# Kernel optimization log

Hardware: AMD Instinct MI355X
Metric: run time of the kernel (lower is better)

Reference implementation:

```python
import jax, jax.numpy as jnp
import numpy as np

HEAD_SIZE = 64  # EMBEDDING_SIZE(384) // HEAD_NO(6)

def setup_inputs() -> dict:
    key = jax.random.key(0)
    ks = jax.random.split(key, 6)
    B, T, C, H, D = 256, 256, 384, 6, 64
    s = 0.02
    return {
        "x": jax.random.normal(ks[0], (B, T, C), dtype=jnp.float32),
        "Wq": jax.random.normal(ks[1], (H, C, D), dtype=jnp.float32) * s,
        "Wk": jax.random.normal(ks[2], (H, C, D), dtype=jnp.float32) * s,
        "Wv": jax.random.normal(ks[3], (H, C, D), dtype=jnp.float32) * s,
        "Wproj": jax.random.normal(ks[4], (C, C), dtype=jnp.float32) * s,
        "bproj": jnp.zeros((C,), dtype=jnp.float32),
    }

def reference(x, Wq, Wk, Wv, Wproj, bproj):
    B, T, C = x.shape
    # per-head projections, stacked over heads h: [B, H, T, D]
    q = jnp.einsum('btc,hcd->bhtd', x, Wq)
    k = jnp.einsum('btc,hcd->bhtd', x, Wk)
    v = jnp.einsum('btc,hcd->bhtd', x, Wv)
    scale = 1.0 / jnp.sqrt(jnp.asarray(HEAD_SIZE, dtype=x.dtype))
    # scores [B, H, T, T]; causal mask (masked_fill then /scale == scale then mask, since -inf/scale=-inf)
    scores = jnp.einsum('bhtd,bhsd->bhts', q, k) * scale
    causal = jnp.tril(jnp.ones((T, T), dtype=bool))
    scores = jnp.where(causal, scores, -jnp.inf)
    w = jax.nn.softmax(scores, axis=-1)
    # dropout is identity in eval mode
    out = jnp.einsum('bhts,bhsd->bhtd', w, v)          # [B, H, T, D]
    out = out.transpose(0, 2, 1, 3).reshape(B, T, C)    # concat heads -> [B, T, C]
    return out @ Wproj + bproj
```

## Files before the change

kernel.cpp:

```cpp
#include <hip/hip_runtime.h>
#include <hip/hip_bf16.h>

typedef __bf16 bf16;
typedef unsigned int u32;
typedef __attribute__((ext_vector_type(8))) __bf16 bf16x8;
typedef __attribute__((ext_vector_type(4))) float f32x4;

#define Bsz 256
#define Tsz 256
#define Csz 384
#define Hn  6
#define Dh  64
#define NQKV 1152

#define MFMA16(a, b, c) __builtin_amdgcn_mfma_f32_16x16x32_bf16(a, b, c, 0, 0, 0)

typedef __attribute__((address_space(3))) u32 lds_u32;
typedef __attribute__((address_space(1))) const u32 gbl_u32;
__device__ __forceinline__ void gl2lds16(const void* g, void* l) {
    __builtin_amdgcn_global_load_lds((gbl_u32*)g, (lds_u32*)l, 16, 0, 0);
}

__device__ __forceinline__ float redmax16(float x) {
    x = fmaxf(x, __shfl_xor(x, 1));
    x = fmaxf(x, __shfl_xor(x, 2));
    x = fmaxf(x, __shfl_xor(x, 4));
    x = fmaxf(x, __shfl_xor(x, 8));
    return x;
}
__device__ __forceinline__ float redsum16(float x) {
    x += __shfl_xor(x, 1);
    x += __shfl_xor(x, 2);
    x += __shfl_xor(x, 4);
    x += __shfl_xor(x, 8);
    return x;
}

__global__ __launch_bounds__(256) void convert_x(
    const float* __restrict__ x, bf16* __restrict__ xb)
{
    size_t i = ((size_t)blockIdx.x * 256 + threadIdx.x) * 8;
    float4 f0 = *(const float4*)&x[i];
    float4 f1 = *(const float4*)&x[i + 4];
    bf16x8 o;
    o[0] = (bf16)f0.x; o[1] = (bf16)f0.y; o[2] = (bf16)f0.z; o[3] = (bf16)f0.w;
    o[4] = (bf16)f1.x; o[5] = (bf16)f1.y; o[6] = (bf16)f1.z; o[7] = (bf16)f1.w;
    *(bf16x8*)&xb[i] = o;
}

__global__ __launch_bounds__(384) void prep_w(
    const float* __restrict__ Wq, const float* __restrict__ Wk,
    const float* __restrict__ Wv, const float* __restrict__ Wp,
    bf16* __restrict__ Btqkv, bf16* __restrict__ Bpt)
{
    const int n = blockIdx.x, k = threadIdx.x;
    if (n < NQKV) {
        int wi = n / Csz, rem = n - wi * Csz, h = rem >> 6, d = rem & 63;
        const float* W = wi == 0 ? Wq : (wi == 1 ? Wk : Wv);
        Btqkv[(size_t)n * Csz + k] = (bf16)W[((size_t)h * Csz + k) * Dh + d];
    } else {
        int n2 = n - NQKV;
        Bpt[(size_t)n2 * Csz + k] = (bf16)Wp[(size_t)k * Csz + n2];
    }
}


__device__ __forceinline__ void stage_tile(
    const char* Ab, const char* Bb, int m0, int n0, int t,
    bf16 (*As)[256][64], bf16 (*Bs)[128][64], int buf, int tid)
{
    const int srow = tid >> 3;
    const int scs  = ((tid & 7) * 16) ^ (((tid >> 3) & 7) << 4);
    #pragma unroll
    for (int j = 0; j < 8; ++j)
        gl2lds16(Ab + (size_t)(m0 + j * 32 + srow) * 768 + t * 128 + scs,
                 (char*)&As[buf][0][0] + j * 4096 + tid * 16);
    #pragma unroll
    for (int j = 0; j < 4; ++j)
        gl2lds16(Bb + (size_t)(n0 + j * 32 + srow) * 768 + t * 128 + scs,
                 (char*)&Bs[buf][0][0] + j * 4096 + tid * 16);
}

__device__ __forceinline__ void compute_tile(
    const bf16 (*As)[256][64], const bf16 (*Bs)[128][64], int buf,
    int wmw, int wnw, int l4, int quad, f32x4 acc[8][4])
{
    const char* Ap = (const char*)&As[buf][0][0];
    const char* Bp = (const char*)&Bs[buf][0][0];
    const int cswz = (l4 & 7) << 4;
    bf16x8 bfr[4][2];
    #pragma unroll
    for (int fn = 0; fn < 4; ++fn)
        #pragma unroll
        for (int ks = 0; ks < 2; ++ks)
            bfr[fn][ks] = *(const bf16x8*)(Bp + (wnw * 64 + fn * 16 + l4) * 128 +
                                           ((ks * 64 + quad * 16) ^ cswz));
    #pragma unroll
    for (int mh = 0; mh < 2; ++mh) {
        bf16x8 af[4][2];
        #pragma unroll
        for (int fr = 0; fr < 4; ++fr)
            #pragma unroll
            for (int ks = 0; ks < 2; ++ks)
                af[fr][ks] = *(const bf16x8*)(Ap + (wmw * 128 + mh * 64 + fr * 16 + l4) * 128 +
                                              ((ks * 64 + quad * 16) ^ cswz));
        __builtin_amdgcn_s_setprio(1);
        #pragma unroll
        for (int ks = 0; ks < 2; ++ks)
            #pragma unroll
            for (int fr = 0; fr < 4; ++fr)
                #pragma unroll
                for (int fn = 0; fn < 4; ++fn)
                    acc[mh * 4 + fr][fn] = MFMA16(af[fr][ks], bfr[fn][ks], acc[mh * 4 + fr][fn]);
        __builtin_amdgcn_s_setprio(0);
    }
}

#define GEMM_PIPE()                                                            \
    stage_tile(Ab, Bb, m0, n0, 0, As, Bs, 0, tid);                             \
    stage_tile(Ab, Bb, m0, n0, 1, As, Bs, 1, tid);                             \
    asm volatile("s_waitcnt vmcnt(12)" ::: "memory");                          \
    __builtin_amdgcn_s_barrier();                                              \
    _Pragma("unroll")                                                          \
    for (int t = 0; t < 6; ++t) {                                              \
        if (t < 4) stage_tile(Ab, Bb, m0, n0, t + 2, As, Bs, (t + 2) % 3, tid);\
        compute_tile(As, Bs, t % 3, wmw, wnw, l4, quad, acc);                  \
        if (t < 4) {                                                           \
            asm volatile("s_waitcnt vmcnt(12)" ::: "memory");                  \
            __builtin_amdgcn_s_barrier();                                      \
        } else if (t == 4) {                                                   \
            asm volatile("s_waitcnt vmcnt(0)" ::: "memory");                   \
            __builtin_amdgcn_s_barrier();                                      \
        }                                                                      \
    }

__global__ __launch_bounds__(256, 1) void qkv_gemm(
    const bf16* __restrict__ A, const bf16* __restrict__ Bt,
    bf16* __restrict__ q, bf16* __restrict__ k, bf16* __restrict__ v)
{
    __shared__ bf16 As[3][256][64];
    __shared__ bf16 Bs[3][128][64];
    const int tid = threadIdx.x, w = tid >> 6, lane = tid & 63;
    const int l4 = lane & 15, quad = lane >> 4;
    const int wmw = w >> 1, wnw = w & 1;

    const int orig = blockIdx.x;
    const int id = (orig & 7) * 288 + (orig >> 3);
    const int mt_ = id / 9, nt_ = id - mt_ * 9;
    const int m0 = mt_ * 256, n0 = nt_ * 128;

    const char* Ab = (const char*)A;
    const char* Bb = (const char*)Bt;
    f32x4 acc[8][4] = {};

    GEMM_PIPE();

    #pragma unroll
    for (int fn = 0; fn < 4; ++fn) {
        int n = n0 + wnw * 64 + fn * 16 + l4;
        int wi = n / Csz, rem = n - wi * Csz;
        int h = rem >> 6, d = rem & 63;
        bf16* outp = wi == 0 ? q : (wi == 1 ? k : v);
        #pragma unroll
        for (int fr = 0; fr < 8; ++fr)
            #pragma unroll
            for (int r = 0; r < 4; ++r) {
                int m = m0 + wmw * 128 + fr * 16 + quad * 4 + r;
                int b = m >> 8, tt = m & 255;
                outp[(((size_t)(b * Hn + h)) * Tsz + tt) * Dh + d] = (bf16)acc[fr][fn][r];
            }
    }
}

__global__ __launch_bounds__(256, 1) void proj_gemm(
    const bf16* __restrict__ A, const bf16* __restrict__ Bt,
    const float* __restrict__ bias, float* __restrict__ out)
{
    __shared__ bf16 As[3][256][64];
    __shared__ bf16 Bs[3][128][64];
    const int tid = threadIdx.x, w = tid >> 6, lane = tid & 63;
    const int l4 = lane & 15, quad = lane >> 4;
    const int wmw = w >> 1, wnw = w & 1;

    const int orig = blockIdx.x;
    const int id = (orig & 7) * 96 + (orig >> 3);
    const int mt_ = id / 3, nt_ = id - mt_ * 3;
    const int m0 = mt_ * 256, n0 = nt_ * 128;

    const char* Ab = (const char*)A;
    const char* Bb = (const char*)Bt;
    f32x4 acc[8][4] = {};

    GEMM_PIPE();

    #pragma unroll
    for (int fn = 0; fn < 4; ++fn) {
        int n = n0 + wnw * 64 + fn * 16 + l4;
        float bv = bias[n];
        #pragma unroll
        for (int fr = 0; fr < 8; ++fr)
            #pragma unroll
            for (int r = 0; r < 4; ++r) {
                int m = m0 + wmw * 128 + fr * 16 + quad * 4 + r;
                out[(size_t)m * Csz + n] = acc[fr][fn][r] + bv;
            }
    }
}

__global__ __launch_bounds__(256) void attn_mfma(
    const bf16* __restrict__ q, const bf16* __restrict__ k, const bf16* __restrict__ v,
    bf16* __restrict__ att)
{
    __shared__ bf16 Kl[64][72];
    __shared__ bf16 Vt[64][72];
    __shared__ bf16 Pl[4][16][72];
    const float SCL = 0.18033688f;
    const int tid = threadIdx.x, w = tid >> 6, lane = tid & 63;
    const int l4 = lane & 15, quad = lane >> 4;

    const int orig = blockIdx.x;
    const int blk = (orig & 7) * 768 + (orig >> 3);
    const int bh = blk >> 2, qt = blk & 3;
    const int b = bh / Hn, h = bh % Hn;
    const bf16* qb = q + (size_t)bh * Tsz * Dh;
    const bf16* kb = k + (size_t)bh * Tsz * Dh;
    const bf16* vb = v + (size_t)bh * Tsz * Dh;

    const int trow = qt * 64 + w * 16 + l4;
    const bf16x8 qa0 = *(const bf16x8*)&qb[trow * Dh + quad * 8];
    const bf16x8 qa1 = *(const bf16x8*)&qb[trow * Dh + 32 + quad * 8];

    f32x4 o[4] = {f32x4{0,0,0,0}, f32x4{0,0,0,0}, f32x4{0,0,0,0}, f32x4{0,0,0,0}};
    float mrun[4] = {-3.0e38f, -3.0e38f, -3.0e38f, -3.0e38f};
    float lrun[4] = {0.f, 0.f, 0.f, 0.f};

    for (int kt = 0; kt <= qt; ++kt) {
        #pragma unroll
        for (int it = 0; it < 2; ++it) {
            int idx = it * 256 + tid;
            int s = idx >> 3, d8 = (idx & 7) * 8;
            *(bf16x8*)&Kl[s][d8] = *(const bf16x8*)&kb[(kt * 64 + s) * Dh + d8];
        }
        #pragma unroll
        for (int it = 0; it < 2; ++it) {
            int idx = it * 256 + tid;
            int s = idx & 63, d8 = (idx >> 6) * 8;
            bf16x8 vv = *(const bf16x8*)&vb[(kt * 64 + s) * Dh + d8];
            #pragma unroll
            for (int j = 0; j < 8; ++j) Vt[d8 + j][s] = vv[j];
        }
        __syncthreads();

        f32x4 sc[4] = {f32x4{0,0,0,0}, f32x4{0,0,0,0}, f32x4{0,0,0,0}, f32x4{0,0,0,0}};
        #pragma unroll
        for (int nt = 0; nt < 4; ++nt) {
            bf16x8 b0 = *(const bf16x8*)&Kl[nt * 16 + l4][quad * 8];
            bf16x8 b1 = *(const bf16x8*)&Kl[nt * 16 + l4][32 + quad * 8];
            sc[nt] = MFMA16(qa0, b0, sc[nt]);
            sc[nt] = MFMA16(qa1, b1, sc[nt]);
        }

        float mnew[4], alpha[4];
        #pragma unroll
        for (int r = 0; r < 4; ++r) {
            int tg = qt * 64 + w * 16 + quad * 4 + r;
            float mx = mrun[r];
            #pragma unroll
            for (int nt = 0; nt < 4; ++nt) {
                float sv = sc[nt][r] * SCL;
                int sg = kt * 64 + nt * 16 + l4;
                if (sg > tg) sv = -1.0e30f;
                sc[nt][r] = sv;
                mx = fmaxf(mx, sv);
            }
            mx = redmax16(mx);
            mnew[r] = mx;
            alpha[r] = __builtin_amdgcn_exp2f(mrun[r] - mx);
            mrun[r] = mx;
        }
        #pragma unroll
        for (int r = 0; r < 4; ++r) {
            float sm = 0.f;
            #pragma unroll
            for (int nt = 0; nt < 4; ++nt) {
                float e = __builtin_amdgcn_exp2f(sc[nt][r] - mnew[r]);
                sc[nt][r] = e;
                sm += e;
            }
            sm = redsum16(sm);
            lrun[r] = lrun[r] * alpha[r] + sm;
        }
        #pragma unroll
        for (int nt = 0; nt < 4; ++nt)
            #pragma unroll
            for (int r = 0; r < 4; ++r) o[nt][r] *= alpha[r];

        #pragma unroll
        for (int nt = 0; nt < 4; ++nt)
            #pragma unroll
            for (int r = 0; r < 4; ++r)
                Pl[w][quad * 4 + r][nt * 16 + l4] = (bf16)sc[nt][r];

        bf16x8 pa0 = *(const bf16x8*)&Pl[w][l4][quad * 8];
        bf16x8 pa1 = *(const bf16x8*)&Pl[w][l4][32 + quad * 8];
        #pragma unroll
        for (int nt = 0; nt < 4; ++nt) {
            bf16x8 vb0 = *(const bf16x8*)&Vt[nt * 16 + l4][quad * 8];
            bf16x8 vb1 = *(const bf16x8*)&Vt[nt * 16 + l4][32 + quad * 8];
            o[nt] = MFMA16(pa0, vb0, o[nt]);
            o[nt] = MFMA16(pa1, vb1, o[nt]);
        }
        __syncthreads();
    }

    #pragma unroll
    for (int r = 0; r < 4; ++r) {
        float inv = 1.f / lrun[r];
        int tg = qt * 64 + w * 16 + quad * 4 + r;
        #pragma unroll
        for (int nt = 0; nt < 4; ++nt)
            att[((size_t)(b * Tsz + tg)) * Csz + h * Dh + nt * 16 + l4] =
                (bf16)(o[nt][r] * inv);
    }
}

extern "C" void kernel_launch(void* const* d_in, const int* in_sizes, int n_in,
                              void* d_out, int out_size, void* d_ws, size_t ws_size,
                              hipStream_t stream)
{
    const float* x  = (const float*)d_in[0];
    const float* Wq = (const float*)d_in[1];
    const float* Wk = (const float*)d_in[2];
    const float* Wv = (const float*)d_in[3];
    const float* Wp = (const float*)d_in[4];
    const float* bp = (const float*)d_in[5];
    float* out = (float*)d_out;

    const size_t npe = (size_t)Bsz * Tsz * Csz;
    bf16* xb    = (bf16*)d_ws;
    bf16* att   = xb;
    bf16* q     = xb + npe;
    bf16* k     = q  + npe;
    bf16* v     = k  + npe;
    bf16* Btqkv = v  + npe;
    bf16* Bpt   = Btqkv + (size_t)NQKV * Csz;

    convert_x<<<npe / 2048, 256, 0, stream>>>(x, xb);
    prep_w<<<NQKV + Csz, 384, 0, stream>>>(Wq, Wk, Wv, Wp, Btqkv, Bpt);
    qkv_gemm<<<(Bsz * Tsz / 256) * (NQKV / 128), 256, 0, stream>>>(xb, Btqkv, q, k, v);
    attn_mfma<<<Bsz * Hn * 4, 256, 0, stream>>>(q, k, v, att);
    proj_gemm<<<(Bsz * Tsz / 256) * (Csz / 128), 256, 0, stream>>>(att, Bpt, bp, out);
}
```

Before: 387.5 us.

## Use 8-wave 512-thread GEMM blocks with double-buffered LDS pipeline

Both the QKV and projection GEMMs now run with 512 threads (8 waves) per 256x128 tile instead of 4. Each wave computes a 64x64 sub-tile, so the accumulator array is halved. The LDS pipeline drops from triple to double buffering, which cuts shared memory to 96KB and permits two blocks per CU. The aim is more waves in flight to hide latency, at the cost of an extra barrier per k-step and less prefetch depth.

```diff
diff --git a/kernel.cpp b/kernel.cpp
--- a/kernel.cpp
+++ b/kernel.cpp
@@ -65,84 +65,76 @@
 }
 
 
-__device__ __forceinline__ void stage_tile(
+__device__ __forceinline__ void stage_tile512(
     const char* Ab, const char* Bb, int m0, int n0, int t,
-    bf16 (*As)[256][64], bf16 (*Bs)[128][64], int buf, int tid)
+    char* AsB, char* BsB, int tid)
 {
     const int srow = tid >> 3;
-    const int scs  = ((tid & 7) * 16) ^ (((tid >> 3) & 7) << 4);
-    #pragma unroll
-    for (int j = 0; j < 8; ++j)
-        gl2lds16(Ab + (size_t)(m0 + j * 32 + srow) * 768 + t * 128 + scs,
-                 (char*)&As[buf][0][0] + j * 4096 + tid * 16);
+    const int scs  = ((tid & 7) * 16) ^ ((srow & 7) << 4);
     #pragma unroll
     for (int j = 0; j < 4; ++j)
-        gl2lds16(Bb + (size_t)(n0 + j * 32 + srow) * 768 + t * 128 + scs,
-                 (char*)&Bs[buf][0][0] + j * 4096 + tid * 16);
-}
-
-__device__ __forceinline__ void compute_tile(
-    const bf16 (*As)[256][64], const bf16 (*Bs)[128][64], int buf,
-    int wmw, int wnw, int l4, int quad, f32x4 acc[8][4])
-{
-    const char* Ap = (const char*)&As[buf][0][0];
-    const char* Bp = (const char*)&Bs[buf][0][0];
+        gl2lds16(Ab + (size_t)(m0 + j * 64 + srow) * 768 + t * 128 + scs,
+                 AsB + j * 8192 + tid * 16);
+    #pragma unroll
+    for (int j = 0; j < 2; ++j)
+        gl2lds16(Bb + (size_t)(n0 + j * 64 + srow) * 768 + t * 128 + scs,
+                 BsB + j * 8192 + tid * 16);
+}
+
+__device__ __forceinline__ void compute_tile512(
+    const char* Ap, const char* Bp,
+    int wm4, int wn2, int l4, int quad, f32x4 acc[4][4])
+{
     const int cswz = (l4 & 7) << 4;
-    bf16x8 bfr[4][2];
+    bf16x8 bfr[4][2], af[4][2];
     #pragma unroll
     for (int fn = 0; fn < 4; ++fn)
         #pragma unroll
         for (int ks = 0; ks < 2; ++ks)
-            bfr[fn][ks] = *(const bf16x8*)(Bp + (wnw * 64 + fn * 16 + l4) * 128 +
+            bfr[fn][ks] = *(const bf16x8*)(Bp + (wn2 * 64 + fn * 16 + l4) * 128 +
                                            ((ks * 64 + quad * 16) ^ cswz));
     #pragma unroll
-    for (int mh = 0; mh < 2; ++mh) {
-        bf16x8 af[4][2];
+    for (int fr = 0; fr < 4; ++fr)
+        #pragma unroll
+        for (int ks = 0; ks < 2; ++ks)
+            af[fr][ks] = *(const bf16x8*)(Ap + (wm4 * 64 + fr * 16 + l4) * 128 +
+                                          ((ks * 64 + quad * 16) ^ cswz));
+    __builtin_amdgcn_s_setprio(1);
+    #pragma unroll
+    for (int ks = 0; ks < 2; ++ks)
         #pragma unroll
         for (int fr = 0; fr < 4; ++fr)
             #pragma unroll
-            for (int ks = 0; ks < 2; ++ks)
-                af[fr][ks] = *(const bf16x8*)(Ap + (wmw * 128 + mh * 64 + fr * 16 + l4) * 128 +
-                                              ((ks * 64 + quad * 16) ^ cswz));
-        __builtin_amdgcn_s_setprio(1);
-        #pragma unroll
-        for (int ks = 0; ks < 2; ++ks)
-            #pragma unroll
-            for (int fr = 0; fr < 4; ++fr)
-                #pragma unroll
-                for (int fn = 0; fn < 4; ++fn)
-                    acc[mh * 4 + fr][fn] = MFMA16(af[fr][ks], bfr[fn][ks], acc[mh * 4 + fr][fn]);
-        __builtin_amdgcn_s_setprio(0);
-    }
-}
-
-#define GEMM_PIPE()                                                            \
-    stage_tile(Ab, Bb, m0, n0, 0, As, Bs, 0, tid);                             \
-    stage_tile(Ab, Bb, m0, n0, 1, As, Bs, 1, tid);                             \
-    asm volatile("s_waitcnt vmcnt(12)" ::: "memory");                          \
-    __builtin_amdgcn_s_barrier();                                              \
+            for (int fn = 0; fn < 4; ++fn)
+                acc[fr][fn] = MFMA16(af[fr][ks], bfr[fn][ks], acc[fr][fn]);
+    __builtin_amdgcn_s_setprio(0);
+}
+
+#define GEMM_PIPE8()                                                           \
+    stage_tile512(Ab, Bb, m0, n0, 0, As0, Bs0, tid);                           \
     _Pragma("unroll")                                                          \
     for (int t = 0; t < 6; ++t) {                                              \
-        if (t < 4) stage_tile(Ab, Bb, m0, n0, t + 2, As, Bs, (t + 2) % 3, tid);\
-        compute_tile(As, Bs, t % 3, wmw, wnw, l4, quad, acc);                  \
-        if (t < 4) {                                                           \
-            asm volatile("s_waitcnt vmcnt(12)" ::: "memory");                  \
-            __builtin_amdgcn_s_barrier();                                      \
-        } else if (t == 4) {                                                   \
-            asm volatile("s_waitcnt vmcnt(0)" ::: "memory");                   \
-            __builtin_amdgcn_s_barrier();                                      \
-        }                                                                      \
-    }
-
-__global__ __launch_bounds__(256, 1) void qkv_gemm(
+        if (t < 5) stage_tile512(Ab, Bb, m0, n0, t + 1,                        \
+                                 (t & 1) ? As0 : As1, (t & 1) ? Bs0 : Bs1, tid);\
+        if (t < 5) { asm volatile("s_waitcnt vmcnt(6)" ::: "memory"); }        \
+        else       { asm volatile("s_waitcnt vmcnt(0)" ::: "memory"); }        \
+        __builtin_amdgcn_s_barrier();                                          \
+        compute_tile512((t & 1) ? As1 : As0, (t & 1) ? Bs1 : Bs0,              \
+                        wm4, wn2, l4, quad, acc);                              \
+        __builtin_amdgcn_s_barrier();                                          \
+    }
+
+__global__ __launch_bounds__(512, 2) void qkv_gemm(
     const bf16* __restrict__ A, const bf16* __restrict__ Bt,
     bf16* __restrict__ q, bf16* __restrict__ k, bf16* __restrict__ v)
 {
-    __shared__ bf16 As[3][256][64];
-    __shared__ bf16 Bs[3][128][64];
+    __shared__ bf16 As[2][256][64];
+    __shared__ bf16 Bs[2][128][64];
+    char* As0 = (char*)&As[0][0][0]; char* As1 = (char*)&As[1][0][0];
+    char* Bs0 = (char*)&Bs[0][0][0]; char* Bs1 = (char*)&Bs[1][0][0];
     const int tid = threadIdx.x, w = tid >> 6, lane = tid & 63;
     const int l4 = lane & 15, quad = lane >> 4;
-    const int wmw = w >> 1, wnw = w & 1;
+    const int wm4 = w >> 1, wn2 = w & 1;
 
     const int orig = blockIdx.x;
     const int id = (orig & 7) * 288 + (orig >> 3);
@@ -151,36 +143,38 @@
 
     const char* Ab = (const char*)A;
     const char* Bb = (const char*)Bt;
-    f32x4 acc[8][4] = {};
-
-    GEMM_PIPE();
+    f32x4 acc[4][4] = {};
+
+    GEMM_PIPE8();
 
     #pragma unroll
     for (int fn = 0; fn < 4; ++fn) {
-        int n = n0 + wnw * 64 + fn * 16 + l4;
+        int n = n0 + wn2 * 64 + fn * 16 + l4;
         int wi = n / Csz, rem = n - wi * Csz;
         int h = rem >> 6, d = rem & 63;
         bf16* outp = wi == 0 ? q : (wi == 1 ? k : v);
         #pragma unroll
-        for (int fr = 0; fr < 8; ++fr)
+        for (int fr = 0; fr < 4; ++fr)
             #pragma unroll
             for (int r = 0; r < 4; ++r) {
-                int m = m0 + wmw * 128 + fr * 16 + quad * 4 + r;
+                int m = m0 + wm4 * 64 + fr * 16 + quad * 4 + r;
                 int b = m >> 8, tt = m & 255;
                 outp[(((size_t)(b * Hn + h)) * Tsz + tt) * Dh + d] = (bf16)acc[fr][fn][r];
             }
     }
 }
 
-__global__ __launch_bounds__(256, 1) void proj_gemm(
+__global__ __launch_bounds__(512, 2) void proj_gemm(
     const bf16* __restrict__ A, const bf16* __restrict__ Bt,
     const float* __restrict__ bias, float* __restrict__ out)
 {
-    __shared__ bf16 As[3][256][64];
-    __shared__ bf16 Bs[3][128][64];
+    __shared__ bf16 As[2][256][64];
+    __shared__ bf16 Bs[2][128][64];
+    char* As0 = (char*)&As[0][0][0]; char* As1 = (char*)&As[1][0][0];
+    char* Bs0 = (char*)&Bs[0][0][0]; char* Bs1 = (char*)&Bs[1][0][0];
     const int tid = threadIdx.x, w = tid >> 6, lane = tid & 63;
     const int l4 = lane & 15, quad = lane >> 4;
-    const int wmw = w >> 1, wnw = w & 1;
+    const int wm4 = w >> 1, wn2 = w & 1;
 
     const int orig = blockIdx.x;
     const int id = (orig & 7) * 96 + (orig >> 3);
@@ -189,19 +183,19 @@
 
     const char* Ab = (const char*)A;
     const char* Bb = (const char*)Bt;
-    f32x4 acc[8][4] = {};
-
-    GEMM_PIPE();
+    f32x4 acc[4][4] = {};
+
+    GEMM_PIPE8();
 
     #pragma unroll
     for (int fn = 0; fn < 4; ++fn) {
-        int n = n0 + wnw * 64 + fn * 16 + l4;
+        int n = n0 + wn2 * 64 + fn * 16 + l4;
         float bv = bias[n];
         #pragma unroll
-        for (int fr = 0; fr < 8; ++fr)
+        for (int fr = 0; fr < 4; ++fr)
             #pragma unroll
             for (int r = 0; r < 4; ++r) {
-                int m = m0 + wmw * 128 + fr * 16 + quad * 4 + r;
+                int m = m0 + wm4 * 64 + fr * 16 + quad * 4 + r;
                 out[(size_t)m * Csz + n] = acc[fr][fn][r] + bv;
             }
     }
@@ -347,7 +341,7 @@
 
     convert_x<<<npe / 2048, 256, 0, stream>>>(x, xb);
     prep_w<<<NQKV + Csz, 384, 0, stream>>>(Wq, Wk, Wv, Wp, Btqkv, Bpt);
-    qkv_gemm<<<(Bsz * Tsz / 256) * (NQKV / 128), 256, 0, stream>>>(xb, Btqkv, q, k, v);
+    qkv_gemm<<<(Bsz * Tsz / 256) * (NQKV / 128), 512, 0, stream>>>(xb, Btqkv, q, k, v);
     attn_mfma<<<Bsz * Hn * 4, 256, 0, stream>>>(q, k, v, att);
-    proj_gemm<<<(Bsz * Tsz / 256) * (Csz / 128), 256, 0, stream>>>(att, Bpt, bp, out);
-}
+    proj_gemm<<<(Bsz * Tsz / 256) * (Csz / 128), 512, 0, stream>>>(att, Bpt, bp, out);
+}
```

Result: no change. 388.6 us (+0.3%).
